# Kernel optimization log

Measured on AMD Instinct MI355X. Metric: run time of the kernel, lower is better.

Reference implementation:

```python
import jax, jax.numpy as jnp
import numpy as np

N_HEAD = 8
DIM_K = 64
DIM_MODEL = N_HEAD * DIM_K  # 512; must equal seq_len for the final batch_dot
SCALE = DIM_K ** 0.5


def setup_inputs() -> dict:
    key = jax.random.key(0)
    ks = jax.random.split(key, 4)
    B, S, D_IN = 32, 512, 128
    x = jax.random.normal(ks[0], (B, S, D_IN), dtype=jnp.float32)
    init = 0.02
    Wq = jax.random.normal(ks[1], (D_IN * N_HEAD, DIM_MODEL), dtype=jnp.float32) * init
    Wk = jax.random.normal(ks[2], (D_IN * N_HEAD, DIM_MODEL), dtype=jnp.float32) * init
    Wv = jax.random.normal(ks[3], (D_IN * N_HEAD, DIM_MODEL), dtype=jnp.float32) * init
    z = jnp.zeros((DIM_MODEL,), dtype=jnp.float32)
    return {"x": x, "Wq": Wq, "bq": z, "Wk": Wk, "bk": z, "Wv": Wv, "bv": z}


def reference(x, Wq, bq, Wk, bk, Wv, bv):
    # Tile input n_head times along feature dim (matches K.concatenate([q]*n_head))
    xt = jnp.concatenate([x] * N_HEAD, axis=-1)          # [B, S, d_in*n_head]
    q = xt @ Wq + bq                                      # [B, S, dim_model]
    k = xt @ Wk + bk
    v = xt @ Wv + bv
    # K.batch_dot(q, k, axes=[-1,-1]) -> q @ k^T per batch
    scores = jnp.einsum('bsd,btd->bst', q, k) / SCALE     # [B, S, S]
    attn = jax.nn.softmax(scores, axis=-1)
    # K.batch_dot(v, attn, axes=[2,-1]): out[b,i,j] = sum_k v[b,i,k]*attn[b,j,k]
    # (only valid because S == dim_model, as in the original buggy layer)
    out = jnp.einsum('bik,bjk->bij', v, attn)             # [B, S, S]
    return out
```

## Files before the change

### kernel.cpp

```cpp
#include <hip/hip_runtime.h>


typedef unsigned short u16;
typedef __attribute__((ext_vector_type(8))) short bf16x8;
typedef __attribute__((ext_vector_type(4))) float f32x4;
typedef __attribute__((ext_vector_type(2))) float f32x2;
typedef __attribute__((ext_vector_type(2))) unsigned int u32x2;

__device__ inline u16 f2bf(float f) {
  unsigned u = __float_as_uint(f);
  u = u + 0x7fffu + ((u >> 16) & 1u);
  return (u16)(u >> 16);
}
__device__ inline float bf2f(u16 h) { return __uint_as_float(((unsigned)h) << 16); }

__device__ inline void gl16(const u16* g, u16* l) {
  __builtin_amdgcn_global_load_lds(
      (const __attribute__((address_space(1))) unsigned int*)g,
      (__attribute__((address_space(3))) unsigned int*)l, 16, 0, 0);
}

__global__ __launch_bounds__(256)
void prep_w(const float* __restrict__ Wq, const float* __restrict__ Wk,
            const float* __restrict__ Wv,
            u16* __restrict__ WTh, u16* __restrict__ WTl) {
  __shared__ float sm[128][17];
  int t  = blockIdx.x >> 5;
  int nb = blockIdx.x & 31;
  const float* W = (t == 0) ? Wq : (t == 1) ? Wk : Wv;
  int n0 = nb << 4;
  int nl = threadIdx.x & 15;
  int kq = threadIdx.x >> 4;
  float s[8];
#pragma unroll
  for (int i = 0; i < 8; ++i) s[i] = 0.f;
#pragma unroll
  for (int h = 0; h < 8; ++h)
#pragma unroll
    for (int i = 0; i < 8; ++i)
      s[i] += W[(h * 128 + kq + (i << 4)) * 512 + n0 + nl];
#pragma unroll
  for (int i = 0; i < 8; ++i) sm[kq + (i << 4)][nl] = s[i];
  __syncthreads();
  int no = threadIdx.x >> 4;
  int k8 = (threadIdx.x & 15) << 3;
  bf16x8 h8, l8;
#pragma unroll
  for (int c = 0; c < 8; ++c) {
    float v = sm[k8 + c][no];
    u16 h = f2bf(v);
    h8[c] = (short)h;
    l8[c] = (short)f2bf(v - bf2f(h));
  }
  long o = (long)t * 65536 + (long)(n0 + no) * 128 + k8;
  *(bf16x8*)&WTh[o] = h8;
  *(bf16x8*)&WTl[o] = l8;
}

__global__ __launch_bounds__(256)
void split_x(const float* __restrict__ x, u16* __restrict__ xh, u16* __restrict__ xl) {
  int i = blockIdx.x * 256 + threadIdx.x;
  const f32x4* xx = (const f32x4*)x;
  f32x4 a = xx[i * 2], b = xx[i * 2 + 1];
  float v[8] = {a[0], a[1], a[2], a[3], b[0], b[1], b[2], b[3]};
  bf16x8 h8, l8;
#pragma unroll
  for (int j = 0; j < 8; ++j) {
    u16 h = f2bf(v[j]);
    h8[j] = (short)h;
    l8[j] = (short)f2bf(v[j] - bf2f(h));
  }
  ((bf16x8*)xh)[i] = h8;
  ((bf16x8*)xl)[i] = l8;
}

__global__ __launch_bounds__(256, 2)
void proj_fused(const u16* __restrict__ xh, const u16* __restrict__ xl,
                const u16* __restrict__ WTh, const u16* __restrict__ WTl,
                u16* __restrict__ Qh, u16* __restrict__ Kh, u16* __restrict__ Vh,
                const float* __restrict__ bq, const float* __restrict__ bk,
                const float* __restrict__ bv) {
  __shared__ __align__(16) char ldsraw[65536];
  u16* st = (u16*)ldsraw;

  int tid = threadIdx.x;
  int bid = blockIdx.x;
  bid = (bid & 7) * 192 + (bid >> 3);
  int which = bid % 3;
  int tile  = bid / 3;
  int mt = tile >> 2;
  int nt = tile & 3;

  const u16* Ah = xh + (long)mt * (128 * 128);
  const u16* Al = xl + (long)mt * (128 * 128);
  const u16* Bh = WTh + which * 65536 + nt * 16384;
  const u16* Bl = WTl + which * 65536 + nt * 16384;
  const float* bias = (which == 0) ? bq : (which == 1) ? bk : bv;
  u16* C = (which == 0) ? Qh : (which == 1) ? Kh : Vh;

  int lane = tid & 63;
  int wv = tid >> 6;
  int wm = (wv >> 1) << 6;
  int wn = (wv & 1) << 6;
  int frow = lane & 15;
  int fk = (lane >> 4) << 3;

  f32x4 acc[4][4];
#pragma unroll
  for (int i = 0; i < 4; ++i)
#pragma unroll
    for (int j = 0; j < 4; ++j) {
      f32x4 z = {0.f, 0.f, 0.f, 0.f};
      acc[i][j] = z;
    }

  for (int kk = 0; kk < 2; ++kk) {
    int k0 = kk << 6;
#pragma unroll
    for (int j = 0; j < 4; ++j) {
      int c = j * 256 + tid;
      int row = c >> 3;
      int scol = ((c & 7) ^ (row & 7)) << 3;
      int ga = row * 128 + k0 + scol;
      int lo = c << 3;
      gl16(Ah + ga, st + lo);
      gl16(Al + ga, st + 8192 + lo);
      gl16(Bh + ga, st + 16384 + lo);
      gl16(Bl + ga, st + 24576 + lo);
    }
    __syncthreads();
#pragma unroll
    for (int ks = 0; ks < 2; ++ks) {
      int kb = (ks << 5) + fk;
      bf16x8 a_h[4], a_l[4], b_h[4], b_l[4];
#pragma unroll
      for (int i = 0; i < 4; ++i) {
        int ar = wm + (i << 4) + frow;
        int ao = ar * 64 + (kb ^ ((ar & 7) << 3));
        a_h[i] = *(const bf16x8*)&st[ao];
        a_l[i] = *(const bf16x8*)&st[8192 + ao];
        int br = wn + (i << 4) + frow;
        int bo = br * 64 + (kb ^ ((br & 7) << 3));
        b_h[i] = *(const bf16x8*)&st[16384 + bo];
        b_l[i] = *(const bf16x8*)&st[24576 + bo];
      }
#pragma unroll
      for (int i = 0; i < 4; ++i)
#pragma unroll
        for (int j = 0; j < 4; ++j) {
          acc[i][j] = __builtin_amdgcn_mfma_f32_16x16x32_bf16(a_h[i], b_h[j], acc[i][j], 0, 0, 0);
          acc[i][j] = __builtin_amdgcn_mfma_f32_16x16x32_bf16(a_l[i], b_h[j], acc[i][j], 0, 0, 0);
          acc[i][j] = __builtin_amdgcn_mfma_f32_16x16x32_bf16(a_h[i], b_l[j], acc[i][j], 0, 0, 0);
        }
    }
    __syncthreads();
  }

  float* tr = ((float*)ldsraw) + wv * 2112;
  int lr = lane >> 3;
  int c8 = (lane & 7) << 3;
  int colbase = (nt << 7) + wn + c8;
  float bb[8];
#pragma unroll
  for (int c = 0; c < 8; ++c) bb[c] = bias[colbase + c];
  long rowg0 = (long)(mt << 7) + wm;
#pragma unroll
  for (int q = 0; q < 2; ++q) {
#pragma unroll
    for (int il = 0; il < 2; ++il) {
      int i = (q << 1) + il;
#pragma unroll
      for (int j = 0; j < 4; ++j)
#pragma unroll
        for (int r = 0; r < 4; ++r)
          tr[((il << 4) + ((lane >> 4) << 2) + r) * 66 + (j << 4) + (lane & 15)] =
              acc[i][j][r];
    }
#pragma unroll
    for (int p = 0; p < 4; ++p) {
      int rr = (p << 3) + lr;
      float v[8];
      *(f32x2*)&v[0] = *(const f32x2*)&tr[rr * 66 + c8];
      *(f32x2*)&v[2] = *(const f32x2*)&tr[rr * 66 + c8 + 2];
      *(f32x2*)&v[4] = *(const f32x2*)&tr[rr * 66 + c8 + 4];
      *(f32x2*)&v[6] = *(const f32x2*)&tr[rr * 66 + c8 + 6];
      bf16x8 o8;
#pragma unroll
      for (int c = 0; c < 8; ++c) o8[c] = (short)f2bf(v[c] + bb[c]);
      *(bf16x8*)&C[(rowg0 + (q << 5) + rr) * 512 + colbase] = o8;
    }
  }
}

__global__ __launch_bounds__(256, 2)
void attn_fused(const u16* __restrict__ Q, const u16* __restrict__ K,
                const u16* __restrict__ V, float* __restrict__ OUT) {
  __shared__ __align__(16) char LDS[67584];
  u16* stg = (u16*)LDS;
  u16* qt  = (u16*)(LDS + 32768);
  float* smax = (float*)(LDS + 32768);
  float* ssum = (float*)(LDS + 33280);
  char* Pb = LDS + 34816;

  int tid = threadIdx.x;
  int p = blockIdx.x;
  int xcd = p & 7, sq = p >> 3;
  int b  = (xcd << 2) + (sq >> 4);
  int jb = sq & 15;

  const u16* Qp = Q + ((long)b * 512 + jb * 32) * 512;
  const u16* Kp = K + (long)b * 262144;
  const u16* Vp = V + (long)b * 262144;

  int lane = tid & 63, nw = tid >> 6;
  int frow = lane & 15, hi4 = lane >> 4;

  auto stageKV = [&](const u16* src, int k0) {
#pragma unroll
    for (int j = 0; j < 8; ++j) {
      int c = (j << 8) + tid;
      int row = c >> 2, cc = c & 3;
      int sc = (cc ^ ((row >> 1) & 3)) << 3;
      gl16(src + (long)row * 512 + k0 + sc, stg + (c << 3));
    }
  };
  auto stageQ = [&](int k0) {
    if (tid < 128) {
      int row = tid >> 2, cc = tid & 3;
      int sc = (cc ^ ((row >> 1) & 3)) << 3;
      gl16(Qp + (long)row * 512 + k0 + sc, qt + (tid << 3));
    }
  };

  f32x4 acc[8][2];
#pragma unroll
  for (int j = 0; j < 8; ++j)
#pragma unroll
    for (int i = 0; i < 2; ++i) {
      f32x4 z = {0.f, 0.f, 0.f, 0.f};
      acc[j][i] = z;
    }

  stageKV(Kp, 0);
  stageQ(0);

  for (int kk = 0; kk < 16; ++kk) {
    __syncthreads();
    bf16x8 a[8], bq_[2];
#pragma unroll
    for (int j = 0; j < 8; ++j) {
      int R = (nw << 7) + (j << 4) + frow;
      int cc = hi4 ^ ((R >> 1) & 3);
      a[j] = *(const bf16x8*)&stg[(R << 5) + (cc << 3)];
    }
#pragma unroll
    for (int i = 0; i < 2; ++i) {
      int R = (i << 4) + frow;
      int cc = hi4 ^ ((R >> 1) & 3);
      bq_[i] = *(const bf16x8*)&qt[(R << 5) + (cc << 3)];
    }
    __syncthreads();
    if (kk < 15) {
      int k0 = (kk + 1) << 5;
      stageKV(Kp, k0);
      stageQ(k0);
    } else {
      stageKV(Vp, 0);
    }
#pragma unroll
    for (int j = 0; j < 8; ++j)
#pragma unroll
      for (int i = 0; i < 2; ++i)
        acc[j][i] = __builtin_amdgcn_mfma_f32_16x16x32_bf16(a[j], bq_[i], acc[j][i], 0, 0, 0);
  }

  float mx[2];
#pragma unroll
  for (int i = 0; i < 2; ++i) {
    float m = acc[0][i][0];
#pragma unroll
    for (int j = 0; j < 8; ++j)
#pragma unroll
      for (int r = 0; r < 4; ++r) m = fmaxf(m, acc[j][i][r]);
    m = fmaxf(m, __shfl_xor(m, 16));
    m = fmaxf(m, __shfl_xor(m, 32));
    mx[i] = m;
  }
  if (hi4 == 0) {
#pragma unroll
    for (int i = 0; i < 2; ++i) smax[(((i << 4) + frow) << 2) + nw] = mx[i];
  }
  __syncthreads();
  float mf[2], sm_[2];
#pragma unroll
  for (int i = 0; i < 2; ++i) {
    f32x4 m4 = *(const f32x4*)&smax[((i << 4) + frow) << 2];
    mf[i] = fmaxf(fmaxf(m4[0], m4[1]), fmaxf(m4[2], m4[3]));
    sm_[i] = 0.f;
  }
#pragma unroll
  for (int j = 0; j < 8; ++j)
#pragma unroll
    for (int i = 0; i < 2; ++i)
#pragma unroll
      for (int r = 0; r < 4; ++r) {
        float pv = __expf((acc[j][i][r] - mf[i]) * 0.125f);
        acc[j][i][r] = pv;
        sm_[i] += pv;
      }
#pragma unroll
  for (int i = 0; i < 2; ++i) {
    sm_[i] += __shfl_xor(sm_[i], 16);
    sm_[i] += __shfl_xor(sm_[i], 32);
  }
  if (hi4 == 0) {
#pragma unroll
    for (int i = 0; i < 2; ++i) ssum[(((i << 4) + frow) << 2) + nw] = sm_[i];
  }
  __syncthreads();
  float inv_[2];
#pragma unroll
  for (int i = 0; i < 2; ++i) {
    f32x4 s4 = *(const f32x4*)&ssum[((i << 4) + frow) << 2];
    inv_[i] = 1.f / (s4[0] + s4[1] + s4[2] + s4[3]);
  }
#pragma unroll
  for (int i = 0; i < 2; ++i) {
    int qrow = (i << 4) + frow;
#pragma unroll
    for (int j = 0; j < 8; ++j) {
      int col0 = (nw << 7) + (j << 4) + (hi4 << 2);
      unsigned lo = (unsigned)f2bf(acc[j][i][0] * inv_[i]) |
                    ((unsigned)f2bf(acc[j][i][1] * inv_[i]) << 16);
      unsigned hi = (unsigned)f2bf(acc[j][i][2] * inv_[i]) |
                    ((unsigned)f2bf(acc[j][i][3] * inv_[i]) << 16);
      u32x2 w = {lo, hi};
      int byt = ((qrow << 10) + (col0 << 1)) ^ ((qrow & 7) << 4);
      *(u32x2*)(Pb + byt) = w;
    }
  }
  __syncthreads();

  f32x4 o[8][2];
#pragma unroll
  for (int j = 0; j < 8; ++j)
#pragma unroll
    for (int i = 0; i < 2; ++i) {
      f32x4 z = {0.f, 0.f, 0.f, 0.f};
      o[j][i] = z;
    }

  for (int kk = 0; kk < 16; ++kk) {
    if (kk) __syncthreads();
    int k0 = kk << 5;
    bf16x8 av[8], bp[2];
#pragma unroll
    for (int j = 0; j < 8; ++j) {
      int R = (nw << 7) + (j << 4) + frow;
      int cc = hi4 ^ ((R >> 1) & 3);
      av[j] = *(const bf16x8*)&stg[(R << 5) + (cc << 3)];
    }
#pragma unroll
    for (int i = 0; i < 2; ++i) {
      int R = (i << 4) + frow;
      int byt = ((R << 10) + ((k0 + (hi4 << 3)) << 1)) ^ ((R & 7) << 4);
      bp[i] = *(const bf16x8*)(Pb + byt);
    }
    __syncthreads();
    if (kk < 15) stageKV(Vp, (kk + 1) << 5);
#pragma unroll
    for (int j = 0; j < 8; ++j)
#pragma unroll
      for (int i = 0; i < 2; ++i)
        o[j][i] = __builtin_amdgcn_mfma_f32_16x16x32_bf16(av[j], bp[i], o[j][i], 0, 0, 0);
  }

  float* Ob = OUT + (long)b * 262144 + jb * 32;
#pragma unroll
  for (int j = 0; j < 8; ++j)
#pragma unroll
    for (int i = 0; i < 2; ++i)
#pragma unroll
      for (int r = 0; r < 4; ++r) {
        int vrow = (nw << 7) + (j << 4) + (hi4 << 2) + r;
        Ob[(long)vrow * 512 + (i << 4) + frow] = o[j][i][r];
      }
}

extern "C" void kernel_launch(void* const* d_in, const int* in_sizes, int n_in,
                              void* d_out, int out_size, void* d_ws, size_t ws_size,
                              hipStream_t stream) {
  const float* x  = (const float*)d_in[0];
  const float* Wq = (const float*)d_in[1];
  const float* bq = (const float*)d_in[2];
  const float* Wk = (const float*)d_in[3];
  const float* bk = (const float*)d_in[4];
  const float* Wv = (const float*)d_in[5];
  const float* bv = (const float*)d_in[6];
  float* out = (float*)d_out;

  char* ws = (char*)d_ws;
  size_t off = 0;
  auto alloc = [&](size_t bytes) -> char* {
    char* p = ws + off;
    off = (off + bytes + 255) & ~(size_t)255;
    return p;
  };
  u16* WTh = (u16*)alloc((size_t)3 * 512 * 128 * 2);
  u16* WTl = (u16*)alloc((size_t)3 * 512 * 128 * 2);
  u16* xh  = (u16*)alloc((size_t)16384 * 128 * 2);
  u16* xl  = (u16*)alloc((size_t)16384 * 128 * 2);
  u16* Qh  = (u16*)alloc((size_t)16384 * 512 * 2);
  u16* Kh  = (u16*)alloc((size_t)16384 * 512 * 2);
  u16* Vh  = (u16*)alloc((size_t)16384 * 512 * 2);

  prep_w<<<96, 256, 0, stream>>>(Wq, Wk, Wv, WTh, WTl);
  split_x<<<1024, 256, 0, stream>>>(x, xh, xl);
  proj_fused<<<1536, 256, 0, stream>>>(xh, xl, WTh, WTl, Qh, Kh, Vh, bq, bk, bv);
  attn_fused<<<512, 256, 0, stream>>>(Qh, Kh, Vh, out);
}
```

Baseline: 95.27 us.

## Load K/V fragments directly from global with register double-buffering, 512-thread blocks

The attention kernel now stages the whole 32-row Q tile into LDS once and reads K and V MFMA fragments straight from global memory into registers, double-buffered across k-steps. This removes the per-step LDS staging of K/V and its barriers. Blocks double to 512 threads (8 waves, 64 rows each), which halves per-wave accumulators and raises the occupancy hint. The cost is uncoalesced 16-byte global reads for K/V that depend on the L2 cache, and an LDS footprint that is still about 66 KB per block.

```diff
diff --git a/kernel.cpp b/kernel.cpp
--- a/kernel.cpp
+++ b/kernel.cpp
@@ -192,21 +192,20 @@
   }
 }
 
-__global__ __launch_bounds__(256, 2)
+__global__ __launch_bounds__(512, 4)
 void attn_fused(const u16* __restrict__ Q, const u16* __restrict__ K,
                 const u16* __restrict__ V, float* __restrict__ OUT) {
   __shared__ __align__(16) char LDS[67584];
-  u16* stg = (u16*)LDS;
-  u16* qt  = (u16*)(LDS + 32768);
-  float* smax = (float*)(LDS + 32768);
-  float* ssum = (float*)(LDS + 33280);
-  char* Pb = LDS + 34816;
+  u16* QT = (u16*)LDS;
+  char* Pb = LDS + 32768;
+  float* smax = (float*)(LDS + 65536);
+  float* ssum = (float*)(LDS + 66560);
 
   int tid = threadIdx.x;
   int p = blockIdx.x;
-  int xcd = p & 7, sq = p >> 3;
-  int b  = (xcd << 2) + (sq >> 4);
-  int jb = sq & 15;
+  int xcd = p & 7, idx = p >> 3;
+  int b  = (xcd << 2) + (idx >> 4);
+  int jb = idx & 15;
 
   const u16* Qp = Q + ((long)b * 512 + jb * 32) * 512;
   const u16* Kp = K + (long)b * 262144;
@@ -214,176 +213,191 @@
 
   int lane = tid & 63, nw = tid >> 6;
   int frow = lane & 15, hi4 = lane >> 4;
-
-  auto stageKV = [&](const u16* src, int k0) {
-#pragma unroll
-    for (int j = 0; j < 8; ++j) {
-      int c = (j << 8) + tid;
-      int row = c >> 2, cc = c & 3;
-      int sc = (cc ^ ((row >> 1) & 3)) << 3;
-      gl16(src + (long)row * 512 + k0 + sc, stg + (c << 3));
-    }
+  int R0 = (nw << 6) + frow;
+
+#pragma unroll
+  for (int j = 0; j < 4; ++j) {
+    int u = (j << 9) + tid;
+    int row = u >> 6, sl = u & 63;
+    gl16(Qp + (long)row * 512 + ((sl ^ (row & 7)) << 3), QT + (u << 3));
+  }
+
+  auto rq = [&](int row, int s) -> bf16x8 {
+    return *(const bf16x8*)&QT[(row << 9) + ((s ^ (row & 7)) << 3)];
   };
-  auto stageQ = [&](int k0) {
-    if (tid < 128) {
-      int row = tid >> 2, cc = tid & 3;
-      int sc = (cc ^ ((row >> 1) & 3)) << 3;
-      gl16(Qp + (long)row * 512 + k0 + sc, qt + (tid << 3));
-    }
+  auto lda_ = [&](const u16* base, int R, int s) -> bf16x8 {
+    return *(const bf16x8*)(base + ((long)R << 9) + (s << 3));
   };
-
-  f32x4 acc[8][2];
-#pragma unroll
-  for (int j = 0; j < 8; ++j)
-#pragma unroll
-    for (int i = 0; i < 2; ++i) {
+  auto rp = [&](int row, int s) -> bf16x8 {
+    return *(const bf16x8*)(Pb + (row << 10) + ((s ^ (row & 7)) << 4));
+  };
+
+  f32x4 acc[4][2];
+#pragma unroll
+  for (int jj = 0; jj < 4; ++jj)
+#pragma unroll
+    for (int ii = 0; ii < 2; ++ii) {
       f32x4 z = {0.f, 0.f, 0.f, 0.f};
-      acc[j][i] = z;
-    }
-
-  stageKV(Kp, 0);
-  stageQ(0);
-
-  for (int kk = 0; kk < 16; ++kk) {
-    __syncthreads();
-    bf16x8 a[8], bq_[2];
-#pragma unroll
-    for (int j = 0; j < 8; ++j) {
-      int R = (nw << 7) + (j << 4) + frow;
-      int cc = hi4 ^ ((R >> 1) & 3);
-      a[j] = *(const bf16x8*)&stg[(R << 5) + (cc << 3)];
-    }
-#pragma unroll
-    for (int i = 0; i < 2; ++i) {
-      int R = (i << 4) + frow;
-      int cc = hi4 ^ ((R >> 1) & 3);
-      bq_[i] = *(const bf16x8*)&qt[(R << 5) + (cc << 3)];
-    }
-    __syncthreads();
-    if (kk < 15) {
-      int k0 = (kk + 1) << 5;
-      stageKV(Kp, k0);
-      stageQ(k0);
-    } else {
-      stageKV(Vp, 0);
-    }
-#pragma unroll
-    for (int j = 0; j < 8; ++j)
-#pragma unroll
-      for (int i = 0; i < 2; ++i)
-        acc[j][i] = __builtin_amdgcn_mfma_f32_16x16x32_bf16(a[j], bq_[i], acc[j][i], 0, 0, 0);
-  }
-
-  float mx[2];
-#pragma unroll
-  for (int i = 0; i < 2; ++i) {
-    float m = acc[0][i][0];
-#pragma unroll
-    for (int j = 0; j < 8; ++j)
-#pragma unroll
-      for (int r = 0; r < 4; ++r) m = fmaxf(m, acc[j][i][r]);
+      acc[jj][ii] = z;
+    }
+
+  bf16x8 kf0[4], kf1[4];
+#pragma unroll
+  for (int jj = 0; jj < 4; ++jj) kf0[jj] = lda_(Kp, R0 + (jj << 4), hi4);
+  __syncthreads();
+
+  for (int k = 0; k < 8; ++k) {
+    int s0 = (k << 3) + hi4;
+#pragma unroll
+    for (int jj = 0; jj < 4; ++jj) kf1[jj] = lda_(Kp, R0 + (jj << 4), s0 + 4);
+    {
+      bf16x8 q0[2];
+#pragma unroll
+      for (int ii = 0; ii < 2; ++ii) q0[ii] = rq((ii << 4) + frow, s0);
+#pragma unroll
+      for (int jj = 0; jj < 4; ++jj)
+#pragma unroll
+        for (int ii = 0; ii < 2; ++ii)
+          acc[jj][ii] = __builtin_amdgcn_mfma_f32_16x16x32_bf16(kf0[jj], q0[ii], acc[jj][ii], 0, 0, 0);
+    }
+    if (k < 7) {
+#pragma unroll
+      for (int jj = 0; jj < 4; ++jj) kf0[jj] = lda_(Kp, R0 + (jj << 4), s0 + 8);
+    }
+    {
+      bf16x8 q1[2];
+#pragma unroll
+      for (int ii = 0; ii < 2; ++ii) q1[ii] = rq((ii << 4) + frow, s0 + 4);
+#pragma unroll
+      for (int jj = 0; jj < 4; ++jj)
+#pragma unroll
+        for (int ii = 0; ii < 2; ++ii)
+          acc[jj][ii] = __builtin_amdgcn_mfma_f32_16x16x32_bf16(kf1[jj], q1[ii], acc[jj][ii], 0, 0, 0);
+    }
+  }
+
+  bf16x8 vf0[4], vf1[4];
+#pragma unroll
+  for (int jj = 0; jj < 4; ++jj) vf0[jj] = lda_(Vp, R0 + (jj << 4), hi4);
+
+  float mx[2], sm[2], inv_[2];
+#pragma unroll
+  for (int ii = 0; ii < 2; ++ii) {
+    float m = acc[0][ii][0];
+#pragma unroll
+    for (int jj = 0; jj < 4; ++jj)
+#pragma unroll
+      for (int r = 0; r < 4; ++r) m = fmaxf(m, acc[jj][ii][r]);
     m = fmaxf(m, __shfl_xor(m, 16));
     m = fmaxf(m, __shfl_xor(m, 32));
-    mx[i] = m;
+    mx[ii] = m;
   }
   if (hi4 == 0) {
 #pragma unroll
-    for (int i = 0; i < 2; ++i) smax[(((i << 4) + frow) << 2) + nw] = mx[i];
+    for (int ii = 0; ii < 2; ++ii) smax[(((ii << 4) + frow) << 3) + nw] = mx[ii];
   }
   __syncthreads();
-  float mf[2], sm_[2];
-#pragma unroll
-  for (int i = 0; i < 2; ++i) {
-    f32x4 m4 = *(const f32x4*)&smax[((i << 4) + frow) << 2];
-    mf[i] = fmaxf(fmaxf(m4[0], m4[1]), fmaxf(m4[2], m4[3]));
-    sm_[i] = 0.f;
-  }
-#pragma unroll
-  for (int j = 0; j < 8; ++j)
-#pragma unroll
-    for (int i = 0; i < 2; ++i)
+#pragma unroll
+  for (int ii = 0; ii < 2; ++ii) {
+    f32x4 a = *(const f32x4*)&smax[((ii << 4) + frow) << 3];
+    f32x4 c = *(const f32x4*)&smax[((((ii << 4) + frow) << 3) + 4)];
+    mx[ii] = fmaxf(fmaxf(fmaxf(a[0], a[1]), fmaxf(a[2], a[3])),
+                   fmaxf(fmaxf(c[0], c[1]), fmaxf(c[2], c[3])));
+    sm[ii] = 0.f;
+  }
+#pragma unroll
+  for (int jj = 0; jj < 4; ++jj)
+#pragma unroll
+    for (int ii = 0; ii < 2; ++ii)
 #pragma unroll
       for (int r = 0; r < 4; ++r) {
-        float pv = __expf((acc[j][i][r] - mf[i]) * 0.125f);
-        acc[j][i][r] = pv;
-        sm_[i] += pv;
+        float pv = __expf((acc[jj][ii][r] - mx[ii]) * 0.125f);
+        acc[jj][ii][r] = pv;
+        sm[ii] += pv;
       }
 #pragma unroll
-  for (int i = 0; i < 2; ++i) {
-    sm_[i] += __shfl_xor(sm_[i], 16);
-    sm_[i] += __shfl_xor(sm_[i], 32);
+  for (int ii = 0; ii < 2; ++ii) {
+    sm[ii] += __shfl_xor(sm[ii], 16);
+    sm[ii] += __shfl_xor(sm[ii], 32);
   }
   if (hi4 == 0) {
 #pragma unroll
-    for (int i = 0; i < 2; ++i) ssum[(((i << 4) + frow) << 2) + nw] = sm_[i];
+    for (int ii = 0; ii < 2; ++ii) ssum[(((ii << 4) + frow) << 3) + nw] = sm[ii];
   }
   __syncthreads();
-  float inv_[2];
-#pragma unroll
-  for (int i = 0; i < 2; ++i) {
-    f32x4 s4 = *(const f32x4*)&ssum[((i << 4) + frow) << 2];
-    inv_[i] = 1.f / (s4[0] + s4[1] + s4[2] + s4[3]);
-  }
-#pragma unroll
-  for (int i = 0; i < 2; ++i) {
-    int qrow = (i << 4) + frow;
-#pragma unroll
-    for (int j = 0; j < 8; ++j) {
-      int col0 = (nw << 7) + (j << 4) + (hi4 << 2);
-      unsigned lo = (unsigned)f2bf(acc[j][i][0] * inv_[i]) |
-                    ((unsigned)f2bf(acc[j][i][1] * inv_[i]) << 16);
-      unsigned hi = (unsigned)f2bf(acc[j][i][2] * inv_[i]) |
-                    ((unsigned)f2bf(acc[j][i][3] * inv_[i]) << 16);
+#pragma unroll
+  for (int ii = 0; ii < 2; ++ii) {
+    f32x4 a = *(const f32x4*)&ssum[((ii << 4) + frow) << 3];
+    f32x4 c = *(const f32x4*)&ssum[((((ii << 4) + frow) << 3) + 4)];
+    inv_[ii] = 1.f / (a[0] + a[1] + a[2] + a[3] + c[0] + c[1] + c[2] + c[3]);
+  }
+#pragma unroll
+  for (int ii = 0; ii < 2; ++ii) {
+    int qr = (ii << 4) + frow;
+    int rowoff = qr << 10;
+    int swz = (qr & 7) << 4;
+#pragma unroll
+    for (int jj = 0; jj < 4; ++jj) {
+      int c0 = ((nw << 6) + (jj << 4) + (hi4 << 2)) << 1;
+      unsigned lo = (unsigned)f2bf(acc[jj][ii][0] * inv_[ii]) |
+                    ((unsigned)f2bf(acc[jj][ii][1] * inv_[ii]) << 16);
+      unsigned hi = (unsigned)f2bf(acc[jj][ii][2] * inv_[ii]) |
+                    ((unsigned)f2bf(acc[jj][ii][3] * inv_[ii]) << 16);
       u32x2 w = {lo, hi};
-      int byt = ((qrow << 10) + (col0 << 1)) ^ ((qrow & 7) << 4);
-      *(u32x2*)(Pb + byt) = w;
+      *(u32x2*)(Pb + ((rowoff + c0) ^ swz)) = w;
     }
   }
   __syncthreads();
 
-  f32x4 o[8][2];
-#pragma unroll
-  for (int j = 0; j < 8; ++j)
-#pragma unroll
-    for (int i = 0; i < 2; ++i) {
+  f32x4 o[4][2];
+#pragma unroll
+  for (int jj = 0; jj < 4; ++jj)
+#pragma unroll
+    for (int ii = 0; ii < 2; ++ii) {
       f32x4 z = {0.f, 0.f, 0.f, 0.f};
-      o[j][i] = z;
-    }
-
-  for (int kk = 0; kk < 16; ++kk) {
-    if (kk) __syncthreads();
-    int k0 = kk << 5;
-    bf16x8 av[8], bp[2];
-#pragma unroll
-    for (int j = 0; j < 8; ++j) {
-      int R = (nw << 7) + (j << 4) + frow;
-      int cc = hi4 ^ ((R >> 1) & 3);
-      av[j] = *(const bf16x8*)&stg[(R << 5) + (cc << 3)];
-    }
-#pragma unroll
-    for (int i = 0; i < 2; ++i) {
-      int R = (i << 4) + frow;
-      int byt = ((R << 10) + ((k0 + (hi4 << 3)) << 1)) ^ ((R & 7) << 4);
-      bp[i] = *(const bf16x8*)(Pb + byt);
-    }
-    __syncthreads();
-    if (kk < 15) stageKV(Vp, (kk + 1) << 5);
-#pragma unroll
-    for (int j = 0; j < 8; ++j)
-#pragma unroll
-      for (int i = 0; i < 2; ++i)
-        o[j][i] = __builtin_amdgcn_mfma_f32_16x16x32_bf16(av[j], bp[i], o[j][i], 0, 0, 0);
+      o[jj][ii] = z;
+    }
+
+  for (int k = 0; k < 8; ++k) {
+    int s0 = (k << 3) + hi4;
+#pragma unroll
+    for (int jj = 0; jj < 4; ++jj) vf1[jj] = lda_(Vp, R0 + (jj << 4), s0 + 4);
+    {
+      bf16x8 p0[2];
+#pragma unroll
+      for (int ii = 0; ii < 2; ++ii) p0[ii] = rp((ii << 4) + frow, s0);
+#pragma unroll
+      for (int jj = 0; jj < 4; ++jj)
+#pragma unroll
+        for (int ii = 0; ii < 2; ++ii)
+          o[jj][ii] = __builtin_amdgcn_mfma_f32_16x16x32_bf16(vf0[jj], p0[ii], o[jj][ii], 0, 0, 0);
+    }
+    if (k < 7) {
+#pragma unroll
+      for (int jj = 0; jj < 4; ++jj) vf0[jj] = lda_(Vp, R0 + (jj << 4), s0 + 8);
+    }
+    {
+      bf16x8 p1[2];
+#pragma unroll
+      for (int ii = 0; ii < 2; ++ii) p1[ii] = rp((ii << 4) + frow, s0 + 4);
+#pragma unroll
+      for (int jj = 0; jj < 4; ++jj)
+#pragma unroll
+        for (int ii = 0; ii < 2; ++ii)
+          o[jj][ii] = __builtin_amdgcn_mfma_f32_16x16x32_bf16(vf1[jj], p1[ii], o[jj][ii], 0, 0, 0);
+    }
   }
 
   float* Ob = OUT + (long)b * 262144 + jb * 32;
 #pragma unroll
-  for (int j = 0; j < 8; ++j)
-#pragma unroll
-    for (int i = 0; i < 2; ++i)
+  for (int jj = 0; jj < 4; ++jj)
+#pragma unroll
+    for (int ii = 0; ii < 2; ++ii)
 #pragma unroll
       for (int r = 0; r < 4; ++r) {
-        int vrow = (nw << 7) + (j << 4) + (hi4 << 2) + r;
-        Ob[(long)vrow * 512 + (i << 4) + frow] = o[j][i][r];
+        int vrow = (nw << 6) + (jj << 4) + (hi4 << 2) + r;
+        int qc = (ii << 4) + frow;
+        Ob[(long)vrow * 512 + qc] = o[jj][ii][r];
       }
 }
 
@@ -417,5 +431,5 @@
   prep_w<<<96, 256, 0, stream>>>(Wq, Wk, Wv, WTh, WTl);
   split_x<<<1024, 256, 0, stream>>>(x, xh, xl);
   proj_fused<<<1536, 256, 0, stream>>>(xh, xl, WTh, WTl, Qh, Kh, Vh, bq, bk, bv);
-  attn_fused<<<512, 256, 0, stream>>>(Qh, Kh, Vh, out);
-}
+  attn_fused<<<512, 512, 0, stream>>>(Qh, Kh, Vh, out);
+}
```

New measurement: 115.3 us. +21.1%, slower.
